# Kernel tuning notes

Hardware: AMD Instinct MI355X
Metric: run time of the kernel (lower is better)

## Reference

```python
import jax, jax.numpy as jnp
import numpy as np

BN_EPS = 1e-5
TN_EPS = 1e-4


def binarize(x):
    # Clipped straight-through binarization (Courbariaux BNN / Brevitas 1-bit):
    # forward = sign(x) in {-1,+1}, backward = hardtanh STE.
    xc = jnp.clip(x, -1.0, 1.0)
    return xc + jax.lax.stop_gradient(jnp.where(x >= 0, 1.0, -1.0).astype(x.dtype) - xc)


def setup_inputs() -> dict:
    key = jax.random.key(0)
    ks = jax.random.split(key, 20)
    B, D, H, C = 16384, 1024, 1024, 10
    inp = {"x": jax.random.uniform(ks[0], (B, D), dtype=jnp.float32)}
    dims = [(H, D), (H, H), (H, H), (C, H)]
    for i, (o, n) in enumerate(dims):
        inp[f"W{i+1}"] = jax.random.uniform(ks[1 + i], (o, n), minval=-1.0, maxval=1.0, dtype=jnp.float32)
    # BatchNorm1d params (eval mode, running stats) for the 3 hidden layers
    for i in range(3):
        k0, k1, k2, k3 = jax.random.split(ks[5 + i], 4)
        inp[f"g{i+1}"] = 1.0 + 0.1 * jax.random.normal(k0, (H,), dtype=jnp.float32)
        inp[f"b{i+1}"] = 0.1 * jax.random.normal(k1, (H,), dtype=jnp.float32)
        inp[f"m{i+1}"] = 0.1 * jax.random.normal(k2, (H,), dtype=jnp.float32)
        inp[f"v{i+1}"] = 0.5 + jax.random.uniform(k3, (H,), dtype=jnp.float32)
    # TensorNorm (scalar norm on the logits)
    inp["tn_w"] = jnp.ones((), dtype=jnp.float32)
    inp["tn_b"] = jnp.zeros((), dtype=jnp.float32)
    inp["tn_m"] = jnp.zeros((), dtype=jnp.float32)
    inp["tn_v"] = jnp.ones((), dtype=jnp.float32)
    return inp


def reference(x, W1, W2, W3, W4,
              g1, b1, m1, v1,
              g2, b2, m2, v2,
              g3, b3, m3, v3,
              tn_w, tn_b, tn_m, tn_v):
    h = binarize(2.0 * x.reshape(x.shape[0], -1) - 1.0)
    # Dropout is identity in eval mode.
    bn = [(g1, b1, m1, v1), (g2, b2, m2, v2), (g3, b3, m3, v3)]
    for W, (g, b, m, v) in zip((W1, W2, W3), bn):
        h = h @ binarize(W).T                      # [B,H] fake-quant linear, no bias
        h = (h - m) * (g * jax.lax.rsqrt(v + BN_EPS)) + b  # BatchNorm1d eval
        h = binarize(h)                            # 1-bit activation quant
    h = h @ binarize(W4).T                         # [B,10]
    # TensorNorm: scalar affine normalization over the whole tensor
    return (h - tn_m) * jax.lax.rsqrt(tn_v + TN_EPS) * tn_w + tn_b
```

## Files before the change

### kernel.cpp

```cpp
#include <hip/hip_runtime.h>
#include <stdint.h>

typedef int   v4i  __attribute__((ext_vector_type(4)));
typedef int   v8i  __attribute__((ext_vector_type(8)));
typedef float v16f __attribute__((ext_vector_type(16)));
typedef unsigned int uint32;

#define BATCH 16384
#define FEAT  1024

#define OFF_ACTA 0u
#define OFF_ACTB 16777216u
#define OFF_WA1  33554432u
#define OFF_WA2  34603008u
#define OFF_WA3  35651584u
#define OFF_WA4  36700160u
#define OFF_TH   36732928u

__device__ __forceinline__ uint32 nib8(uint32 lo, uint32 hb) {
    uint32 r = 0u;
#pragma unroll
    for (int j = 0; j < 4; ++j) {
        uint32 b = (lo >> (8 * j)) & 0xFFu;
        r |= (((b & 8u) | ((b & 1u) << 1)) << (4 * j));
    }
#pragma unroll
    for (int j = 0; j < 4; ++j) {
        uint32 b = (hb >> (8 * j)) & 0xFFu;
        r |= (((b & 8u) | ((b & 1u) << 1)) << (4 * j + 16));
    }
    return r;
}

__global__ void __launch_bounds__(256) prep_kernel(
    const float* __restrict__ x,
    const float* __restrict__ W1, const float* __restrict__ W2,
    const float* __restrict__ W3, const float* __restrict__ W4,
    const float* __restrict__ g1, const float* __restrict__ b1,
    const float* __restrict__ m1, const float* __restrict__ v1,
    const float* __restrict__ g2, const float* __restrict__ b2,
    const float* __restrict__ m2, const float* __restrict__ v2,
    const float* __restrict__ g3, const float* __restrict__ b3,
    const float* __restrict__ m3, const float* __restrict__ v3,
    char* __restrict__ actA, char* __restrict__ wa1, char* __restrict__ wa2,
    char* __restrict__ wa3, char* __restrict__ wa4, int* __restrict__ TH)
{
    int b = blockIdx.x;
    if (b == 609) {
        for (int gid = threadIdx.x; gid < 3072; gid += 256) {
            int l = gid >> 10, j = gid & 1023;
            const float *g, *bb, *m, *v;
            if (l == 0)      { g = g1; bb = b1; m = m1; v = v1; }
            else if (l == 1) { g = g2; bb = b2; m = m2; v = v2; }
            else             { g = g3; bb = b3; m = m3; v = v3; }
            double gd = (double)g[j], bd = (double)bb[j], md = (double)m[j], vd = (double)v[j];
            double s = gd / sqrt(vd + 1e-5);
            int t2;
            if (s > 0.0)      t2 = (int)ceil(md - bd / s);
            else if (s < 0.0) t2 = -(int)floor(md - bd / s);
            else              t2 = (bd >= 0.0) ? -2000000 : 2000000;
            int sidx = (j >> 5) * 32 + ((j >> 2) & 1) * 16 + (j & 3) + 4 * ((j & 31) >> 3);
            TH[l * 1024 + sidx] = t2;
        }
        return;
    }

    const float* src; char* dst; float thr; int nrows; int dblk;
    const float* gp = nullptr;
    if (b < 512)      { src = x  + (size_t)b * 32768;            dst = actA; dblk = b;      thr = 0.5f; nrows = 32; }
    else if (b < 544) { int mb = b - 512; src = W1 + (size_t)mb * 32768; dst = wa1; dblk = mb; thr = 0.0f; nrows = 32; gp = g1; }
    else if (b < 576) { int mb = b - 544; src = W2 + (size_t)mb * 32768; dst = wa2; dblk = mb; thr = 0.0f; nrows = 32; gp = g2; }
    else if (b < 608) { int mb = b - 576; src = W3 + (size_t)mb * 32768; dst = wa3; dblk = mb; thr = 0.0f; nrows = 32; gp = g3; }
    else              { src = W4; dst = wa4; dblk = 0; thr = 0.0f; nrows = 10; }

    __shared__ unsigned char T[32][1040];
#pragma unroll
    for (int u = 0; u < 8; ++u) {
        int unit = threadIdx.x + u * 256;
        int row  = unit >> 6;
        int c16  = (unit & 63) << 4;
        uint32 wb0 = 0, wb1 = 0, wb2 = 0, wb3 = 0;
        if (row < nrows) {
            bool flipb = gp && (gp[dblk * 32 + row] < 0.0f);
            const float* p = src + (size_t)row * 1024 + c16;
            float4 f0 = *(const float4*)(p + 0);
            float4 f1 = *(const float4*)(p + 4);
            float4 f2 = *(const float4*)(p + 8);
            float4 f3 = *(const float4*)(p + 12);
#define BY(f) ((((f) >= thr) != flipb) ? 0x01u : 0xFFu)
            wb0 = BY(f0.x) | (BY(f0.y)<<8) | (BY(f0.z)<<16) | (BY(f0.w)<<24);
            wb1 = BY(f1.x) | (BY(f1.y)<<8) | (BY(f1.z)<<16) | (BY(f1.w)<<24);
            wb2 = BY(f2.x) | (BY(f2.y)<<8) | (BY(f2.z)<<16) | (BY(f2.w)<<24);
            wb3 = BY(f3.x) | (BY(f3.y)<<8) | (BY(f3.z)<<16) | (BY(f3.w)<<24);
#undef BY
        }
        *(uint4*)&T[row][c16] = make_uint4(wb0, wb1, wb2, wb3);
    }
    __syncthreads();

    int lane = threadIdx.x & 63;
    int wq   = threadIdx.x >> 6;
    int c    = lane & 31;
    int hi   = lane >> 5;
#pragma unroll
    for (int u = 0; u < 4; ++u) {
        int f = wq * 4 + u;
        uint32 dw0, dw1, dw2, dw3;
        {
            int base = 64 * f + 4 * hi;
            dw0 = nib8(*(const uint32*)&T[c][base],      *(const uint32*)&T[c][base + 8]);
            dw1 = nib8(*(const uint32*)&T[c][base + 16], *(const uint32*)&T[c][base + 24]);
            dw2 = nib8(*(const uint32*)&T[c][base + 32], *(const uint32*)&T[c][base + 40]);
            dw3 = nib8(*(const uint32*)&T[c][base + 48], *(const uint32*)&T[c][base + 56]);
        }
        *(uint4*)(dst + (((size_t)dblk * 16 + f) * 64 + lane) * 16) = make_uint4(dw0, dw1, dw2, dw3);
    }
}

__device__ __forceinline__ void gload16(const v4i* gsrc, v4i* ldst) {
    __builtin_amdgcn_global_load_lds(
        (const __attribute__((address_space(1))) void*)gsrc,
        (__attribute__((address_space(3))) void*)ldst, 16, 0, 0);
}

__device__ __forceinline__ v16f MFMA4(v4i a, v4i b, v16f c) {
    v8i av; av[0] = a[0]; av[1] = a[1]; av[2] = a[2]; av[3] = a[3];
    av[4] = 0; av[5] = 0; av[6] = 0; av[7] = 0;
    v8i bv; bv[0] = b[0]; bv[1] = b[1]; bv[2] = b[2]; bv[3] = b[3];
    bv[4] = 0; bv[5] = 0; bv[6] = 0; bv[7] = 0;
    return __builtin_amdgcn_mfma_scale_f32_32x32x64_f8f6f4(
        av, bv, c, 4, 4, 0, 0x7F7F7F7F, 0, 0x7F7F7F7F);
}

__global__ void __launch_bounds__(1024, 4) net_kernel(
    const v4i* __restrict__ Xp,  const v4i* __restrict__ Wp1,
    const v4i* __restrict__ Wp2, const v4i* __restrict__ Wp3,
    const v4i* __restrict__ Wp4, const int* __restrict__ TH,
    const float* __restrict__ tw, const float* __restrict__ tb,
    const float* __restrict__ tm, const float* __restrict__ tv,
    float* __restrict__ out)
{
    __shared__ v4i Hs[2048];
    const int tid  = threadIdx.x;
    const int lane = tid & 63;
    const int wv   = tid >> 6;
    const int hi   = lane >> 5;
    const int blk  = blockIdx.x;

    {
        const v4i* src = Xp + (size_t)blk * 2048;
#pragma unroll
        for (int j = 0; j < 2; ++j)
            gload16(src + j * 1024 + wv * 64 + lane, &Hs[j * 1024 + wv * 64]);
    }
    asm volatile("s_waitcnt vmcnt(0)" ::: "memory");
    __syncthreads();

    const int mt0 = wv * 2, mt1 = wv * 2 + 1;
    const int f0s = wv & 15;

#pragma unroll 1
    for (int l = 0; l < 3; ++l) {
        const v4i* W = (l == 0) ? Wp1 : (l == 1) ? Wp2 : Wp3;
        const int* thl = TH + l * 1024;

        v16f acc00, acc01, acc10, acc11;
        {
            const int4* t0 = (const int4*)(thl + mt0 * 32 + hi * 16);
            const int4* t1 = (const int4*)(thl + mt1 * 32 + hi * 16);
#pragma unroll
            for (int g = 0; g < 4; ++g) {
                int4 ta = t0[g], tc = t1[g];
                acc00[4*g+0] = -(float)ta.x; acc00[4*g+1] = -(float)ta.y;
                acc00[4*g+2] = -(float)ta.z; acc00[4*g+3] = -(float)ta.w;
                acc10[4*g+0] = -(float)tc.x; acc10[4*g+1] = -(float)tc.y;
                acc10[4*g+2] = -(float)tc.z; acc10[4*g+3] = -(float)tc.w;
            }
#pragma unroll
            for (int q = 0; q < 16; ++q) { acc01[q] = acc00[q]; acc11[q] = acc10[q]; }
        }

        const v4i* A0 = W + (size_t)mt0 * 16 * 64 + lane;
        const v4i* A1 = W + (size_t)mt1 * 16 * 64 + lane;
#pragma unroll 2
        for (int fs = 0; fs < 16; ++fs) {
            const int f = (fs + f0s) & 15;
            v4i b0 = Hs[f * 64 + lane];
            v4i b1 = Hs[(16 + f) * 64 + lane];
            v4i a0 = A0[f * 64];
            v4i a1 = A1[f * 64];
            acc00 = MFMA4(a0, b0, acc00);
            acc01 = MFMA4(a0, b1, acc01);
            acc10 = MFMA4(a1, b0, acc10);
            acc11 = MFMA4(a1, b1, acc11);
        }

#define NB4(h) (((h) >= 0.0f) ? 2u : 10u)
        uint32 p00a = 0, p00b = 0, p01a = 0, p01b = 0;
        uint32 p10a = 0, p10b = 0, p11a = 0, p11b = 0;
#pragma unroll
        for (int j = 0; j < 8; ++j) {
            p00a |= NB4(acc00[j]) << (4 * j);  p00b |= NB4(acc00[8 + j]) << (4 * j);
            p01a |= NB4(acc01[j]) << (4 * j);  p01b |= NB4(acc01[8 + j]) << (4 * j);
            p10a |= NB4(acc10[j]) << (4 * j);  p10b |= NB4(acc10[8 + j]) << (4 * j);
            p11a |= NB4(acc11[j]) << (4 * j);  p11b |= NB4(acc11[8 + j]) << (4 * j);
        }
#undef NB4

        __syncthreads();
        {
            v4i o;
            o[0] = (int)p00a; o[1] = (int)p00b; o[2] = (int)p10a; o[3] = (int)p10b;
            Hs[(0 * 16 + wv) * 64 + lane] = o;
            o[0] = (int)p01a; o[1] = (int)p01b; o[2] = (int)p11a; o[3] = (int)p11b;
            Hs[(16 + wv) * 64 + lane] = o;
        }
        __syncthreads();
    }

    if (wv < 2) {
        const int nb = wv;
        v16f acc;
#pragma unroll
        for (int z = 0; z < 16; ++z) acc[z] = 0.0f;
#pragma unroll
        for (int f = 0; f < 16; ++f) {
            v4i av = Wp4[f * 64 + lane];
            v4i bv = Hs[(nb * 16 + f) * 64 + lane];
            acc = MFMA4(av, bv, acc);
        }
        double sc  = (double)tw[0] / sqrt((double)tv[0] + 1e-4);
        double off = (double)tb[0] - (double)tm[0] * sc;
        int colg = blk * 64 + nb * 32 + (lane & 31);
#pragma unroll
        for (int q = 0; q < 8; ++q) {
            int rr = (q & 3) + 8 * (q >> 2) + 4 * hi;
            if (rr < 10)
                out[(size_t)colg * 10 + rr] = (float)((double)acc[q] * sc + off);
        }
    }
}

extern "C" void kernel_launch(void* const* d_in, const int* in_sizes, int n_in,
                              void* d_out, int out_size, void* d_ws, size_t ws_size,
                              hipStream_t stream) {
    const float* x  = (const float*)d_in[0];
    const float* W1 = (const float*)d_in[1];
    const float* W2 = (const float*)d_in[2];
    const float* W3 = (const float*)d_in[3];
    const float* W4 = (const float*)d_in[4];
    const float* g1 = (const float*)d_in[5];
    const float* b1 = (const float*)d_in[6];
    const float* m1 = (const float*)d_in[7];
    const float* v1 = (const float*)d_in[8];
    const float* g2 = (const float*)d_in[9];
    const float* b2 = (const float*)d_in[10];
    const float* m2 = (const float*)d_in[11];
    const float* v2 = (const float*)d_in[12];
    const float* g3 = (const float*)d_in[13];
    const float* b3 = (const float*)d_in[14];
    const float* m3 = (const float*)d_in[15];
    const float* v3 = (const float*)d_in[16];
    const float* tw = (const float*)d_in[17];
    const float* tb = (const float*)d_in[18];
    const float* tm = (const float*)d_in[19];
    const float* tv = (const float*)d_in[20];

    char* ws = (char*)d_ws;
    char* actA = ws + OFF_ACTA;
    char* wa1  = ws + OFF_WA1;
    char* wa2  = ws + OFF_WA2;
    char* wa3  = ws + OFF_WA3;
    char* wa4  = ws + OFF_WA4;
    int*  TH   = (int*)(ws + OFF_TH);

    prep_kernel<<<610, 256, 0, stream>>>(x, W1, W2, W3, W4,
                                         g1, b1, m1, v1, g2, b2, m2, v2,
                                         g3, b3, m3, v3,
                                         actA, wa1, wa2, wa3, wa4, TH);

    net_kernel<<<256, 1024, 0, stream>>>((const v4i*)actA,
                                         (const v4i*)wa1, (const v4i*)wa2,
                                         (const v4i*)wa3, (const v4i*)wa4,
                                         TH, tw, tb, tm, tv, (float*)d_out);
}
```

Before: 172.7 us.

## Fuse input binarization and FP4 packing into the main network kernel

Moves binarization of x (threshold at 0.5) and nibble packing out of the prep kernel and into net_kernel. Each block now reads its 64 fp32 rows directly, packs them through an LDS transpose buffer into Hs, and no longer round-trips a packed activation buffer through global memory. The prep kernel shrinks to weight and threshold preparation only. The starting weight-fragment index is also staggered per block to spread weight reads. The cost is about 33KB of extra LDS per block, which may reduce occupancy, plus in-kernel conversion work before the first MFMA.

```diff
diff --git a/kernel.cpp b/kernel.cpp
--- a/kernel.cpp
+++ b/kernel.cpp
@@ -9,8 +9,6 @@
 #define BATCH 16384
 #define FEAT  1024
 
-#define OFF_ACTA 0u
-#define OFF_ACTB 16777216u
 #define OFF_WA1  33554432u
 #define OFF_WA2  34603008u
 #define OFF_WA3  35651584u
@@ -33,7 +31,6 @@
 }
 
 __global__ void __launch_bounds__(256) prep_kernel(
-    const float* __restrict__ x,
     const float* __restrict__ W1, const float* __restrict__ W2,
     const float* __restrict__ W3, const float* __restrict__ W4,
     const float* __restrict__ g1, const float* __restrict__ b1,
@@ -42,11 +39,11 @@
     const float* __restrict__ m2, const float* __restrict__ v2,
     const float* __restrict__ g3, const float* __restrict__ b3,
     const float* __restrict__ m3, const float* __restrict__ v3,
-    char* __restrict__ actA, char* __restrict__ wa1, char* __restrict__ wa2,
+    char* __restrict__ wa1, char* __restrict__ wa2,
     char* __restrict__ wa3, char* __restrict__ wa4, int* __restrict__ TH)
 {
     int b = blockIdx.x;
-    if (b == 609) {
+    if (b == 97) {
         for (int gid = threadIdx.x; gid < 3072; gid += 256) {
             int l = gid >> 10, j = gid & 1023;
             const float *g, *bb, *m, *v;
@@ -65,13 +62,12 @@
         return;
     }
 
-    const float* src; char* dst; float thr; int nrows; int dblk;
+    const float* src; char* dst; int nrows; int dblk;
     const float* gp = nullptr;
-    if (b < 512)      { src = x  + (size_t)b * 32768;            dst = actA; dblk = b;      thr = 0.5f; nrows = 32; }
-    else if (b < 544) { int mb = b - 512; src = W1 + (size_t)mb * 32768; dst = wa1; dblk = mb; thr = 0.0f; nrows = 32; gp = g1; }
-    else if (b < 576) { int mb = b - 544; src = W2 + (size_t)mb * 32768; dst = wa2; dblk = mb; thr = 0.0f; nrows = 32; gp = g2; }
-    else if (b < 608) { int mb = b - 576; src = W3 + (size_t)mb * 32768; dst = wa3; dblk = mb; thr = 0.0f; nrows = 32; gp = g3; }
-    else              { src = W4; dst = wa4; dblk = 0; thr = 0.0f; nrows = 10; }
+    if (b < 32)       { dblk = b;      src = W1 + (size_t)dblk * 32768; dst = wa1; nrows = 32; gp = g1; }
+    else if (b < 64)  { dblk = b - 32; src = W2 + (size_t)dblk * 32768; dst = wa2; nrows = 32; gp = g2; }
+    else if (b < 96)  { dblk = b - 64; src = W3 + (size_t)dblk * 32768; dst = wa3; nrows = 32; gp = g3; }
+    else              { dblk = 0;      src = W4;                        dst = wa4; nrows = 10; }
 
     __shared__ unsigned char T[32][1040];
 #pragma unroll
@@ -87,7 +83,7 @@
             float4 f1 = *(const float4*)(p + 4);
             float4 f2 = *(const float4*)(p + 8);
             float4 f3 = *(const float4*)(p + 12);
-#define BY(f) ((((f) >= thr) != flipb) ? 0x01u : 0xFFu)
+#define BY(f) ((((f) >= 0.0f) != flipb) ? 0x01u : 0xFFu)
             wb0 = BY(f0.x) | (BY(f0.y)<<8) | (BY(f0.z)<<16) | (BY(f0.w)<<24);
             wb1 = BY(f1.x) | (BY(f1.y)<<8) | (BY(f1.z)<<16) | (BY(f1.w)<<24);
             wb2 = BY(f2.x) | (BY(f2.y)<<8) | (BY(f2.z)<<16) | (BY(f2.w)<<24);
@@ -117,12 +113,6 @@
     }
 }
 
-__device__ __forceinline__ void gload16(const v4i* gsrc, v4i* ldst) {
-    __builtin_amdgcn_global_load_lds(
-        (const __attribute__((address_space(1))) void*)gsrc,
-        (__attribute__((address_space(3))) void*)ldst, 16, 0, 0);
-}
-
 __device__ __forceinline__ v16f MFMA4(v4i a, v4i b, v16f c) {
     v8i av; av[0] = a[0]; av[1] = a[1]; av[2] = a[2]; av[3] = a[3];
     av[4] = 0; av[5] = 0; av[6] = 0; av[7] = 0;
@@ -133,31 +123,59 @@
 }
 
 __global__ void __launch_bounds__(1024, 4) net_kernel(
-    const v4i* __restrict__ Xp,  const v4i* __restrict__ Wp1,
-    const v4i* __restrict__ Wp2, const v4i* __restrict__ Wp3,
-    const v4i* __restrict__ Wp4, const int* __restrict__ TH,
+    const float* __restrict__ x,
+    const v4i* __restrict__ Wp1, const v4i* __restrict__ Wp2,
+    const v4i* __restrict__ Wp3, const v4i* __restrict__ Wp4,
+    const int* __restrict__ TH,
     const float* __restrict__ tw, const float* __restrict__ tb,
     const float* __restrict__ tm, const float* __restrict__ tv,
     float* __restrict__ out)
 {
     __shared__ v4i Hs[2048];
+    __shared__ unsigned char T[32][1040];
     const int tid  = threadIdx.x;
     const int lane = tid & 63;
     const int wv   = tid >> 6;
     const int hi   = lane >> 5;
     const int blk  = blockIdx.x;
 
-    {
-        const v4i* src = Xp + (size_t)blk * 2048;
-#pragma unroll
-        for (int j = 0; j < 2; ++j)
-            gload16(src + j * 1024 + wv * 64 + lane, &Hs[j * 1024 + wv * 64]);
-    }
-    asm volatile("s_waitcnt vmcnt(0)" ::: "memory");
-    __syncthreads();
+#pragma unroll 1
+    for (int unit = 0; unit < 2; ++unit) {
+        const float* src = x + ((size_t)blk * 64 + unit * 32) * 1024;
+#pragma unroll
+        for (int u = 0; u < 2; ++u) {
+            int uu  = tid + u * 1024;
+            int row = uu >> 6;
+            int c16 = (uu & 63) << 4;
+            const float* p = src + (size_t)row * 1024 + c16;
+            float4 f0 = *(const float4*)(p + 0);
+            float4 f1 = *(const float4*)(p + 4);
+            float4 f2 = *(const float4*)(p + 8);
+            float4 f3 = *(const float4*)(p + 12);
+#define BY(f) (((f) >= 0.5f) ? 0x01u : 0xFFu)
+            uint32 wb0 = BY(f0.x) | (BY(f0.y)<<8) | (BY(f0.z)<<16) | (BY(f0.w)<<24);
+            uint32 wb1 = BY(f1.x) | (BY(f1.y)<<8) | (BY(f1.z)<<16) | (BY(f1.w)<<24);
+            uint32 wb2 = BY(f2.x) | (BY(f2.y)<<8) | (BY(f2.z)<<16) | (BY(f2.w)<<24);
+            uint32 wb3 = BY(f3.x) | (BY(f3.y)<<8) | (BY(f3.z)<<16) | (BY(f3.w)<<24);
+#undef BY
+            *(uint4*)&T[row][c16] = make_uint4(wb0, wb1, wb2, wb3);
+        }
+        __syncthreads();
+        {
+            int c = lane & 31;
+            int base = 64 * wv + 4 * hi;
+            uint32 dw0 = nib8(*(const uint32*)&T[c][base],      *(const uint32*)&T[c][base + 8]);
+            uint32 dw1 = nib8(*(const uint32*)&T[c][base + 16], *(const uint32*)&T[c][base + 24]);
+            uint32 dw2 = nib8(*(const uint32*)&T[c][base + 32], *(const uint32*)&T[c][base + 40]);
+            uint32 dw3 = nib8(*(const uint32*)&T[c][base + 48], *(const uint32*)&T[c][base + 56]);
+            v4i o; o[0] = (int)dw0; o[1] = (int)dw1; o[2] = (int)dw2; o[3] = (int)dw3;
+            Hs[(unit * 16 + wv) * 64 + lane] = o;
+        }
+        __syncthreads();
+    }
 
     const int mt0 = wv * 2, mt1 = wv * 2 + 1;
-    const int f0s = wv & 15;
+    const int f0s = (wv + blk) & 15;
 
 #pragma unroll 1
     for (int l = 0; l < 3; ++l) {
@@ -267,19 +285,18 @@
     const float* tv = (const float*)d_in[20];
 
     char* ws = (char*)d_ws;
-    char* actA = ws + OFF_ACTA;
     char* wa1  = ws + OFF_WA1;
     char* wa2  = ws + OFF_WA2;
     char* wa3  = ws + OFF_WA3;
     char* wa4  = ws + OFF_WA4;
     int*  TH   = (int*)(ws + OFF_TH);
 
-    prep_kernel<<<610, 256, 0, stream>>>(x, W1, W2, W3, W4,
-                                         g1, b1, m1, v1, g2, b2, m2, v2,
-                                         g3, b3, m3, v3,
-                                         actA, wa1, wa2, wa3, wa4, TH);
-
-    net_kernel<<<256, 1024, 0, stream>>>((const v4i*)actA,
+    prep_kernel<<<98, 256, 0, stream>>>(W1, W2, W3, W4,
+                                        g1, b1, m1, v1, g2, b2, m2, v2,
+                                        g3, b3, m3, v3,
+                                        wa1, wa2, wa3, wa4, TH);
+
+    net_kernel<<<256, 1024, 0, stream>>>(x,
                                          (const v4i*)wa1, (const v4i*)wa2,
                                          (const v4i*)wa3, (const v4i*)wa4,
                                          TH, tw, tb, tm, tv, (float*)d_out);
```

Result: no change. 171.8 us (-0.5%).
